# Kernel tuning notes

Hardware: AMD Instinct MI355X
Metric: run time of the kernel (lower is better)

## Reference

```python
import jax, jax.numpy as jnp
import numpy as np

B, D, H, C = 512, 1024, 512, 4


def setup_inputs() -> dict:
    key = jax.random.key(0)
    k_x, k_v, k_w = jax.random.split(key, 3)
    # x holds categorical values in [0, C) used as float multipliers
    x = jax.random.randint(k_x, (B, D), 0, C).astype(jnp.float32)
    # xavier_normal_ per torch fan computation: V fan_in=D*C, fan_out=H*C; W fan_in=D, fan_out=H
    V = jax.random.normal(k_v, (H, D, C), jnp.float32) * np.float32(np.sqrt(2.0 / (D * C + H * C)))
    b = jnp.zeros((D, C), jnp.float32)
    W = jax.random.normal(k_w, (H, D), jnp.float32) * np.float32(np.sqrt(2.0 / (D + H)))
    c = jnp.zeros((1, H), jnp.float32)
    return {"x": x, "V": V, "b": b, "W": W, "c": c}


def _nade_forward(x, V, b, W, c):
    Bsz = x.shape[0]
    a0 = jnp.broadcast_to(c, (Bsz, c.shape[1]))  # [B, H]
    # per-step slices stacked along leading D axis for lax.scan
    xs = (jnp.transpose(V, (1, 0, 2)),  # [D, H, C]
          b,                            # [D, C]
          W.T,                          # [D, H]
          x.T)                          # [D, B]

    def step(a, inp):
        V_d, b_d, w_d, x_d = inp
        h = jax.nn.sigmoid(a)                 # [B, H]
        logits = h @ V_d + b_d                # [B, C]
        p = jax.nn.log_softmax(logits, axis=1)
        a_new = a + x_d[:, None] * w_d[None, :]  # rank-1 update of running preactivation
        return a_new, (logits, p)

    _, (logits, p) = jax.lax.scan(step, a0, xs)   # each [D, B, C]
    y_hat = jnp.transpose(logits, (1, 0, 2)).reshape(Bsz, -1)  # [B, D*C], d-major blocks of size C
    p_hat = jnp.transpose(p, (1, 0, 2)).reshape(Bsz, -1)
    return y_hat, p_hat


def reference(x, V, b, W, c):
    return _nade_forward(x, V, b, W, c)
```

## Files before the change

### kernel.cpp

```cpp
#include <hip/hip_runtime.h>


#define Bv 512
#define Dv 1024
#define Hv 512
#define Cv 4
#define Kv 32
#define DCv 32

#define L2E 1.4426950408889634f
#define LN2 0.6931471805599453f

typedef __attribute__((ext_vector_type(8))) short short8;
typedef __attribute__((ext_vector_type(4))) float f32x4;

__device__ __forceinline__ float fexp2(float x) { return __builtin_amdgcn_exp2f(x); }
__device__ __forceinline__ float flog2(float x) { return __builtin_amdgcn_logf(x); }
__device__ __forceinline__ float frcp(float x)  { return __builtin_amdgcn_rcpf(x); }

__device__ __forceinline__ unsigned bf16pk(float lo, float hi) {
    return __builtin_amdgcn_perm(__float_as_uint(hi), __float_as_uint(lo), 0x07060302u);
}
__device__ __forceinline__ unsigned short bf16rne(float f) {
    unsigned u = __float_as_uint(f);
    return (unsigned short)((u + 0x7FFFu + ((u >> 16) & 1u)) >> 16);
}

__global__ __launch_bounds__(256) void k_prep(const float* __restrict__ W,
                                              const float* __restrict__ x,
                                              float* __restrict__ WtL,
                                              float* __restrict__ xt) {
    __shared__ float t[64][65];
    const int mb   = blockIdx.x >> 7;
    const int tile = blockIdx.x & 127;
    const int tr   = tile >> 4;
    const int tc   = tile & 15;
    const float* src = mb ? x : W;
    float* dst       = mb ? xt : WtL;
    const float scale = mb ? 1.0f : L2E;
    const int lx = threadIdx.x & 15;
    const int ly = threadIdx.x >> 4;

#pragma unroll
    for (int r = 0; r < 64; r += 16) {
        int row = r + ly;
        float4 v = *(const float4*)(src + (size_t)(tr * 64 + row) * Dv + tc * 64 + lx * 4);
        t[row][lx * 4 + 0] = v.x;
        t[row][lx * 4 + 1] = v.y;
        t[row][lx * 4 + 2] = v.z;
        t[row][lx * 4 + 3] = v.w;
    }
    __syncthreads();
#pragma unroll
    for (int r = 0; r < 64; r += 16) {
        int row = r + ly;
        float4 o = make_float4(t[lx * 4 + 0][row] * scale,
                               t[lx * 4 + 1][row] * scale,
                               t[lx * 4 + 2][row] * scale,
                               t[lx * 4 + 3][row] * scale);
        *(float4*)(dst + (size_t)(tc * 64 + row) * 512 + tr * 64 + lx * 4) = o;
    }
}

__global__ __launch_bounds__(256) void k_prepv(const float* __restrict__ V,
                                               unsigned short* __restrict__ VtA4) {
    __shared__ unsigned short tile[4 * 16 * 16 * 8];
    const int d0 = blockIdx.x * 4;
    const int dd = threadIdx.x & 3;
    const int hb0 = threadIdx.x >> 2;
#pragma unroll
    for (int p = 0; p < 8; ++p) {
        int h = p * 64 + hb0;
        float4 v = *(const float4*)(V + ((size_t)h * Dv + d0 + dd) * Cv);
        int hb = h >> 5, q = (h >> 3) & 3, j = h & 7;
        int base = ((dd * 16 + hb) * 16 + q * 4) * 8 + j;
        tile[base + 0 * 8] = bf16rne(v.x);
        tile[base + 1 * 8] = bf16rne(v.y);
        tile[base + 2 * 8] = bf16rne(v.z);
        tile[base + 3 * 8] = bf16rne(v.w);
    }
    __syncthreads();
    uint4* dst = (uint4*)(VtA4 + (size_t)d0 * 2048);
    const uint4* src = (const uint4*)tile;
    for (int tt = threadIdx.x; tt < 1024; tt += 256) dst[tt] = src[tt];
}

__global__ __launch_bounds__(512) void k_partial(const float* __restrict__ x,
                          const float* __restrict__ WtL, float* __restrict__ A0) {
    int k  = blockIdx.x >> 6;
    int bg = blockIdx.x & 63;
    int h  = threadIdx.x;
    int d0 = k * DCv;

    __shared__ float xs[DCv * 8];
    if (threadIdx.x < DCv * 8) {
        int g = threadIdx.x >> 5;
        int j = threadIdx.x & 31;
        xs[j * 8 + g] = x[(size_t)(bg * 8 + g) * Dv + d0 + j];
    }
    __syncthreads();

    float acc[8];
#pragma unroll
    for (int g = 0; g < 8; ++g) acc[g] = 0.0f;

    const float* wp = WtL + (size_t)d0 * Hv + h;
    for (int j = 0; j < DCv; ++j) {
        float wv = wp[(size_t)j * Hv];
        const float4 x0 = *(const float4*)(xs + j * 8);
        const float4 x1 = *(const float4*)(xs + j * 8 + 4);
        acc[0] = fmaf(x0.x, wv, acc[0]);
        acc[1] = fmaf(x0.y, wv, acc[1]);
        acc[2] = fmaf(x0.z, wv, acc[2]);
        acc[3] = fmaf(x0.w, wv, acc[3]);
        acc[4] = fmaf(x1.x, wv, acc[4]);
        acc[5] = fmaf(x1.y, wv, acc[5]);
        acc[6] = fmaf(x1.z, wv, acc[6]);
        acc[7] = fmaf(x1.w, wv, acc[7]);
    }
#pragma unroll
    for (int g = 0; g < 8; ++g)
        A0[((size_t)k * Bv + bg * 8 + g) * Hv + h] = acc[g];
}

__global__ void k_prefix(float* __restrict__ A0, const float* __restrict__ cbias) {
    int gid = blockIdx.x * blockDim.x + threadIdx.x;
    int h = gid & (Hv - 1);
    int bi = gid >> 9;
    float run = cbias[h] * L2E;
    float* p = A0 + (size_t)bi * Hv + h;
    for (int k = 0; k < Kv; ++k) {
        float t = p[(size_t)k * Bv * Hv];
        p[(size_t)k * Bv * Hv] = run;
        run += t;
    }
}

__global__ __launch_bounds__(256, 4) void k_main(
        const float* __restrict__ xt, const float* __restrict__ bbias,
        const unsigned short* __restrict__ VtA4, const float* __restrict__ WtL,
        const float* __restrict__ A0, float* __restrict__ out) {
    const int k    = blockIdx.x >> 5;
    const int bg   = blockIdx.x & 31;
    const int wid  = threadIdx.x >> 6;
    const int lane = threadIdx.x & 63;
    const int bl   = lane & 15;
    const int quad = lane >> 4;
    const int b    = bg * 16 + bl;
    const int d0   = k * DCv;
    const int stp  = wid >> 1;
    const bool isP = wid & 1;

    __shared__ f32x4 red[2][2][4][64];

    float a[32];
    {
        const float* ap = A0 + ((size_t)k * Bv + b) * Hv + wid * 128 + quad * 8;
#pragma unroll
        for (int kb = 0; kb < 4; ++kb) {
            float4 t0 = *(const float4*)(ap + kb * 32);
            float4 t1 = *(const float4*)(ap + kb * 32 + 4);
            a[kb*8+0]=t0.x; a[kb*8+1]=t0.y; a[kb*8+2]=t0.z; a[kb*8+3]=t0.w;
            a[kb*8+4]=t1.x; a[kb*8+5]=t1.y; a[kb*8+6]=t1.z; a[kb*8+7]=t1.w;
        }
    }

    const bool act = (bl < 4);
    const unsigned short* vp = VtA4 + (((size_t)d0 * 16 + wid * 4) * 16 + quad * 4 + bl) * 8;
    const float* wp = WtL + (size_t)d0 * Hv + wid * 128 + quad * 8;
    const float* xp = xt + (size_t)d0 * Bv + b;
    const float* bp = bbias + (d0 + stp) * Cv;
    float* sp = out + (isP ? (size_t)Bv * Dv * Cv : (size_t)0)
                    + (size_t)b * Dv * Cv + (d0 + stp) * Cv;

    const short8 zfrag = {0,0,0,0,0,0,0,0};

    for (int i1 = 0; i1 < DCv / 2; ++i1) {
        short8 afA[4], afB[4];
#pragma unroll
        for (int kb = 0; kb < 4; ++kb)
            afA[kb] = act ? *(const short8*)(vp + kb * 128) : zfrag;
#pragma unroll
        for (int kb = 0; kb < 4; ++kb)
            afB[kb] = act ? *(const short8*)(vp + 2048 + kb * 128) : zfrag;
        float xdA = xp[0];
        float xdB = xp[Bv];
        float4 bbv = *(const float4*)bp;

        unsigned pkA[16];
#pragma unroll
        for (int m = 0; m < 32; m += 2) {
            float s0 = frcp(1.0f + fexp2(-a[m]));
            float s1 = frcp(1.0f + fexp2(-a[m + 1]));
            pkA[m >> 1] = bf16pk(s0, s1);
        }
        f32x4 accA = {0.f, 0.f, 0.f, 0.f};
#pragma unroll
        for (int kb = 0; kb < 4; ++kb) {
            union { unsigned u[4]; short8 s; } cv;
            cv.u[0] = pkA[kb*4+0]; cv.u[1] = pkA[kb*4+1];
            cv.u[2] = pkA[kb*4+2]; cv.u[3] = pkA[kb*4+3];
            accA = __builtin_amdgcn_mfma_f32_16x16x32_bf16(afA[kb], cv.s, accA, 0, 0, 0);
        }
#pragma unroll
        for (int kb = 0; kb < 4; ++kb)
#pragma unroll
            for (int j = 0; j < 8; ++j)
                a[kb*8+j] = fmaf(xdA, wp[kb*32+j], a[kb*8+j]);

        unsigned pkB[16];
#pragma unroll
        for (int m = 0; m < 32; m += 2) {
            float s0 = frcp(1.0f + fexp2(-a[m]));
            float s1 = frcp(1.0f + fexp2(-a[m + 1]));
            pkB[m >> 1] = bf16pk(s0, s1);
        }
        f32x4 accB = {0.f, 0.f, 0.f, 0.f};
#pragma unroll
        for (int kb = 0; kb < 4; ++kb) {
            union { unsigned u[4]; short8 s; } cv;
            cv.u[0] = pkB[kb*4+0]; cv.u[1] = pkB[kb*4+1];
            cv.u[2] = pkB[kb*4+2]; cv.u[3] = pkB[kb*4+3];
            accB = __builtin_amdgcn_mfma_f32_16x16x32_bf16(afB[kb], cv.s, accB, 0, 0, 0);
        }
#pragma unroll
        for (int kb = 0; kb < 4; ++kb)
#pragma unroll
            for (int j = 0; j < 8; ++j)
                a[kb*8+j] = fmaf(xdB, wp[Hv + kb*32+j], a[kb*8+j]);

        red[i1 & 1][0][wid][lane] = accA;
        red[i1 & 1][1][wid][lane] = accB;
        __syncthreads();

        f32x4 r0 = red[i1 & 1][stp][0][lane];
        f32x4 r1 = red[i1 & 1][stp][1][lane];
        f32x4 r2 = red[i1 & 1][stp][2][lane];
        f32x4 r3 = red[i1 & 1][stp][3][lane];
        float w0 = r0.x + r1.x + r2.x + r3.x + bbv.x;
        float w1 = r0.y + r1.y + r2.y + r3.y + bbv.y;
        float w2 = r0.z + r1.z + r2.z + r3.z + bbv.z;
        float w3 = r0.w + r1.w + r2.w + r3.w + bbv.w;

        if (!isP) {
            if (quad == 0) *(float4*)sp = make_float4(w0, w1, w2, w3);
        } else {
            float mx = fmaxf(fmaxf(w0, w1), fmaxf(w2, w3));
            float e0 = fexp2((w0 - mx) * L2E);
            float e1 = fexp2((w1 - mx) * L2E);
            float e2 = fexp2((w2 - mx) * L2E);
            float e3 = fexp2((w3 - mx) * L2E);
            float lse = mx + flog2(e0 + e1 + e2 + e3) * LN2;
            if (quad == 0)
                *(float4*)sp = make_float4(w0 - lse, w1 - lse, w2 - lse, w3 - lse);
        }

        vp += 2 * 2048;
        wp += 2 * Hv;
        xp += 2 * Bv;
        bp += 2 * Cv;
        sp += 2 * Cv;
    }
}

extern "C" void kernel_launch(void* const* d_in, const int* in_sizes, int n_in,
                              void* d_out, int out_size, void* d_ws, size_t ws_size,
                              hipStream_t stream) {
    const float* x  = (const float*)d_in[0];
    const float* V  = (const float*)d_in[1];
    const float* bb = (const float*)d_in[2];
    const float* W  = (const float*)d_in[3];
    const float* cb = (const float*)d_in[4];
    float* out = (float*)d_out;

    char* ws = (char*)d_ws;
    unsigned short* VtA4 = (unsigned short*)ws;
    float* WtL = (float*)(ws + (size_t)4 * 1024 * 1024);
    float* xt  = (float*)(ws + (size_t)6 * 1024 * 1024);
    float* A0  = (float*)(ws + (size_t)8 * 1024 * 1024);

    k_prep<<<256, 256, 0, stream>>>(W, x, WtL, xt);
    k_prepv<<<Dv / 4, 256, 0, stream>>>(V, VtA4);
    k_partial<<<Kv * (Bv / 8), 512, 0, stream>>>(x, WtL, A0);
    k_prefix<<<(Bv * Hv) / 256, 256, 0, stream>>>(A0, cb);
    k_main<<<Kv * 32, 256, 0, stream>>>(xt, bb, VtA4, WtL, A0, out);
}
```

Baseline: 169.5 us.

## Merge prep kernels, fuse partial+prefix into one state kernel, widen main to 8 waves

Combines the W/x transpose and V repack into a single launch, and replaces the partial-sum plus prefix-scan kernels with one kernel that walks all chunks sequentially per batch group and writes running state directly. The main kernel now uses 512 threads with 8 waves, each owning 64 hidden units instead of 128. This halves per-thread register state and raises occupancy, and the packed float2 FMAs may lower instruction count. In exchange, the state kernel has only 64 blocks, which limits parallelism, and the cross-wave reduction now reads 8 partials instead of 4.

```diff
diff --git a/kernel.cpp b/kernel.cpp
--- a/kernel.cpp
+++ b/kernel.cpp
@@ -13,11 +13,20 @@
 
 typedef __attribute__((ext_vector_type(8))) short short8;
 typedef __attribute__((ext_vector_type(4))) float f32x4;
+typedef __attribute__((ext_vector_type(2))) float v2f;
 
 __device__ __forceinline__ float fexp2(float x) { return __builtin_amdgcn_exp2f(x); }
 __device__ __forceinline__ float flog2(float x) { return __builtin_amdgcn_logf(x); }
 __device__ __forceinline__ float frcp(float x)  { return __builtin_amdgcn_rcpf(x); }
 
+__device__ __forceinline__ v2f fma2(v2f a, v2f b, v2f c) {
+#if __has_builtin(__builtin_elementwise_fma)
+    return __builtin_elementwise_fma(a, b, c);
+#else
+    v2f r; r.x = fmaf(a.x, b.x, c.x); r.y = fmaf(a.y, b.y, c.y); return r;
+#endif
+}
+
 __device__ __forceinline__ unsigned bf16pk(float lo, float hi) {
     return __builtin_amdgcn_perm(__float_as_uint(hi), __float_as_uint(lo), 0x07060302u);
 }
@@ -26,117 +35,105 @@
     return (unsigned short)((u + 0x7FFFu + ((u >> 16) & 1u)) >> 16);
 }
 
-__global__ __launch_bounds__(256) void k_prep(const float* __restrict__ W,
-                                              const float* __restrict__ x,
-                                              float* __restrict__ WtL,
-                                              float* __restrict__ xt) {
-    __shared__ float t[64][65];
-    const int mb   = blockIdx.x >> 7;
-    const int tile = blockIdx.x & 127;
-    const int tr   = tile >> 4;
-    const int tc   = tile & 15;
-    const float* src = mb ? x : W;
-    float* dst       = mb ? xt : WtL;
-    const float scale = mb ? 1.0f : L2E;
-    const int lx = threadIdx.x & 15;
-    const int ly = threadIdx.x >> 4;
-
-#pragma unroll
-    for (int r = 0; r < 64; r += 16) {
-        int row = r + ly;
-        float4 v = *(const float4*)(src + (size_t)(tr * 64 + row) * Dv + tc * 64 + lx * 4);
-        t[row][lx * 4 + 0] = v.x;
-        t[row][lx * 4 + 1] = v.y;
-        t[row][lx * 4 + 2] = v.z;
-        t[row][lx * 4 + 3] = v.w;
+__global__ __launch_bounds__(256) void k_prep_all(
+        const float* __restrict__ V, const float* __restrict__ W,
+        const float* __restrict__ x, unsigned short* __restrict__ VtA4,
+        float* __restrict__ WtL, float* __restrict__ xt) {
+    __shared__ char smem[17408];
+    const int bid = blockIdx.x;
+    if (bid < 256) {
+        unsigned short* tile = (unsigned short*)smem;
+        const int d0 = bid * 4;
+        const int dd = threadIdx.x & 3;
+        const int hb0 = threadIdx.x >> 2;
+#pragma unroll
+        for (int p = 0; p < 8; ++p) {
+            int h = p * 64 + hb0;
+            float4 v = *(const float4*)(V + ((size_t)h * Dv + d0 + dd) * Cv);
+            int hb = h >> 5, q = (h >> 3) & 3, j = h & 7;
+            int base = ((dd * 16 + hb) * 16 + q * 4) * 8 + j;
+            tile[base + 0]  = bf16rne(v.x);
+            tile[base + 8]  = bf16rne(v.y);
+            tile[base + 16] = bf16rne(v.z);
+            tile[base + 24] = bf16rne(v.w);
+        }
+        __syncthreads();
+        uint4* dst = (uint4*)(VtA4 + (size_t)d0 * 2048);
+        const uint4* src = (const uint4*)tile;
+        for (int t = threadIdx.x; t < 1024; t += 256) dst[t] = src[t];
+    } else {
+        float (*t)[65] = (float (*)[65])smem;
+        const int mb   = (bid - 256) >> 7;
+        const int tile = (bid - 256) & 127;
+        const int tr   = tile >> 4;
+        const int tc   = tile & 15;
+        const float* src = mb ? x : W;
+        float* dst       = mb ? xt : WtL;
+        const float scale = mb ? 1.0f : L2E;
+        const int lx = threadIdx.x & 15;
+        const int ly = threadIdx.x >> 4;
+#pragma unroll
+        for (int r = 0; r < 64; r += 16) {
+            int row = r + ly;
+            float4 v = *(const float4*)(src + (size_t)(tr * 64 + row) * Dv + tc * 64 + lx * 4);
+            t[row][lx * 4 + 0] = v.x;
+            t[row][lx * 4 + 1] = v.y;
+            t[row][lx * 4 + 2] = v.z;
+            t[row][lx * 4 + 3] = v.w;
+        }
+        __syncthreads();
+#pragma unroll
+        for (int r = 0; r < 64; r += 16) {
+            int row = r + ly;
+            float4 o = make_float4(t[lx * 4 + 0][row] * scale,
+                                   t[lx * 4 + 1][row] * scale,
+                                   t[lx * 4 + 2][row] * scale,
+                                   t[lx * 4 + 3][row] * scale);
+            *(float4*)(dst + (size_t)(tc * 64 + row) * 512 + tr * 64 + lx * 4) = o;
+        }
+    }
+}
+
+__global__ __launch_bounds__(512) void k_state(
+        const float* __restrict__ x, const float* __restrict__ WtL,
+        const float* __restrict__ cb, float* __restrict__ A0) {
+    __shared__ float xs[Dv * 8];
+    const int bg = blockIdx.x;
+    const int h  = threadIdx.x;
+    for (int idx = threadIdx.x; idx < Dv * 8; idx += 512) {
+        int d = idx & (Dv - 1);
+        int g = idx >> 10;
+        xs[d * 8 + g] = x[(size_t)(bg * 8 + g) * Dv + d];
     }
     __syncthreads();
-#pragma unroll
-    for (int r = 0; r < 64; r += 16) {
-        int row = r + ly;
-        float4 o = make_float4(t[lx * 4 + 0][row] * scale,
-                               t[lx * 4 + 1][row] * scale,
-                               t[lx * 4 + 2][row] * scale,
-                               t[lx * 4 + 3][row] * scale);
-        *(float4*)(dst + (size_t)(tc * 64 + row) * 512 + tr * 64 + lx * 4) = o;
-    }
-}
-
-__global__ __launch_bounds__(256) void k_prepv(const float* __restrict__ V,
-                                               unsigned short* __restrict__ VtA4) {
-    __shared__ unsigned short tile[4 * 16 * 16 * 8];
-    const int d0 = blockIdx.x * 4;
-    const int dd = threadIdx.x & 3;
-    const int hb0 = threadIdx.x >> 2;
-#pragma unroll
-    for (int p = 0; p < 8; ++p) {
-        int h = p * 64 + hb0;
-        float4 v = *(const float4*)(V + ((size_t)h * Dv + d0 + dd) * Cv);
-        int hb = h >> 5, q = (h >> 3) & 3, j = h & 7;
-        int base = ((dd * 16 + hb) * 16 + q * 4) * 8 + j;
-        tile[base + 0 * 8] = bf16rne(v.x);
-        tile[base + 1 * 8] = bf16rne(v.y);
-        tile[base + 2 * 8] = bf16rne(v.z);
-        tile[base + 3 * 8] = bf16rne(v.w);
-    }
-    __syncthreads();
-    uint4* dst = (uint4*)(VtA4 + (size_t)d0 * 2048);
-    const uint4* src = (const uint4*)tile;
-    for (int tt = threadIdx.x; tt < 1024; tt += 256) dst[tt] = src[tt];
-}
-
-__global__ __launch_bounds__(512) void k_partial(const float* __restrict__ x,
-                          const float* __restrict__ WtL, float* __restrict__ A0) {
-    int k  = blockIdx.x >> 6;
-    int bg = blockIdx.x & 63;
-    int h  = threadIdx.x;
-    int d0 = k * DCv;
-
-    __shared__ float xs[DCv * 8];
-    if (threadIdx.x < DCv * 8) {
-        int g = threadIdx.x >> 5;
-        int j = threadIdx.x & 31;
-        xs[j * 8 + g] = x[(size_t)(bg * 8 + g) * Dv + d0 + j];
-    }
-    __syncthreads();
-
-    float acc[8];
-#pragma unroll
-    for (int g = 0; g < 8; ++g) acc[g] = 0.0f;
-
-    const float* wp = WtL + (size_t)d0 * Hv + h;
-    for (int j = 0; j < DCv; ++j) {
-        float wv = wp[(size_t)j * Hv];
-        const float4 x0 = *(const float4*)(xs + j * 8);
-        const float4 x1 = *(const float4*)(xs + j * 8 + 4);
-        acc[0] = fmaf(x0.x, wv, acc[0]);
-        acc[1] = fmaf(x0.y, wv, acc[1]);
-        acc[2] = fmaf(x0.z, wv, acc[2]);
-        acc[3] = fmaf(x0.w, wv, acc[3]);
-        acc[4] = fmaf(x1.x, wv, acc[4]);
-        acc[5] = fmaf(x1.y, wv, acc[5]);
-        acc[6] = fmaf(x1.z, wv, acc[6]);
-        acc[7] = fmaf(x1.w, wv, acc[7]);
-    }
-#pragma unroll
-    for (int g = 0; g < 8; ++g)
-        A0[((size_t)k * Bv + bg * 8 + g) * Hv + h] = acc[g];
-}
-
-__global__ void k_prefix(float* __restrict__ A0, const float* __restrict__ cbias) {
-    int gid = blockIdx.x * blockDim.x + threadIdx.x;
-    int h = gid & (Hv - 1);
-    int bi = gid >> 9;
-    float run = cbias[h] * L2E;
-    float* p = A0 + (size_t)bi * Hv + h;
-    for (int k = 0; k < Kv; ++k) {
-        float t = p[(size_t)k * Bv * Hv];
-        p[(size_t)k * Bv * Hv] = run;
-        run += t;
-    }
-}
-
-__global__ __launch_bounds__(256, 4) void k_main(
+    float cl = cb[h] * L2E;
+    v2f run[4];
+    run[0] = (v2f){cl, cl}; run[1] = (v2f){cl, cl};
+    run[2] = (v2f){cl, cl}; run[3] = (v2f){cl, cl};
+    const float* wp = WtL + h;
+    for (int kk = 0; kk < Kv; ++kk) {
+        float* a0p = A0 + ((size_t)kk * Bv + bg * 8) * Hv + h;
+#pragma unroll
+        for (int t = 0; t < 4; ++t) {
+            a0p[(size_t)(2 * t) * Hv]     = run[t].x;
+            a0p[(size_t)(2 * t + 1) * Hv] = run[t].y;
+        }
+        const float* wkk = wp + (size_t)kk * DCv * Hv;
+#pragma unroll 8
+        for (int j = 0; j < DCv; ++j) {
+            float wv = wkk[(size_t)j * Hv];
+            const float4 xa = *(const float4*)(xs + (kk * DCv + j) * 8);
+            const float4 xb = *(const float4*)(xs + (kk * DCv + j) * 8 + 4);
+            v2f wv2 = {wv, wv};
+            run[0] = fma2((v2f){xa.x, xa.y}, wv2, run[0]);
+            run[1] = fma2((v2f){xa.z, xa.w}, wv2, run[1]);
+            run[2] = fma2((v2f){xb.x, xb.y}, wv2, run[2]);
+            run[3] = fma2((v2f){xb.z, xb.w}, wv2, run[3]);
+        }
+    }
+}
+
+__global__ __launch_bounds__(512, 8) void k_main(
         const float* __restrict__ xt, const float* __restrict__ bbias,
         const unsigned short* __restrict__ VtA4, const float* __restrict__ WtL,
         const float* __restrict__ A0, float* __restrict__ out) {
@@ -148,111 +145,106 @@
     const int quad = lane >> 4;
     const int b    = bg * 16 + bl;
     const int d0   = k * DCv;
-    const int stp  = wid >> 1;
+    const int stp  = (wid >> 1) & 1;
     const bool isP = wid & 1;
-
-    __shared__ f32x4 red[2][2][4][64];
-
-    float a[32];
+    const bool active = wid < 4;
+
+    __shared__ f32x4 red[2][2][8][64];
+
+    v2f a2[8];
     {
-        const float* ap = A0 + ((size_t)k * Bv + b) * Hv + wid * 128 + quad * 8;
-#pragma unroll
-        for (int kb = 0; kb < 4; ++kb) {
-            float4 t0 = *(const float4*)(ap + kb * 32);
-            float4 t1 = *(const float4*)(ap + kb * 32 + 4);
-            a[kb*8+0]=t0.x; a[kb*8+1]=t0.y; a[kb*8+2]=t0.z; a[kb*8+3]=t0.w;
-            a[kb*8+4]=t1.x; a[kb*8+5]=t1.y; a[kb*8+6]=t1.z; a[kb*8+7]=t1.w;
-        }
-    }
-
-    const bool act = (bl < 4);
-    const unsigned short* vp = VtA4 + (((size_t)d0 * 16 + wid * 4) * 16 + quad * 4 + bl) * 8;
-    const float* wp = WtL + (size_t)d0 * Hv + wid * 128 + quad * 8;
+        const float* ap = A0 + ((size_t)k * Bv + b) * Hv + wid * 64 + quad * 8;
+#pragma unroll
+        for (int kb = 0; kb < 2; ++kb)
+#pragma unroll
+            for (int t = 0; t < 4; ++t)
+                a2[kb * 4 + t] = *(const v2f*)(ap + kb * 32 + 2 * t);
+    }
+
+    const int blc = (bl < 4) ? bl : 0;
+    const unsigned short* vp = VtA4 + (((size_t)d0 * 16 + wid * 2) * 16 + quad * 4 + blc) * 8;
+    const float* wp = WtL + (size_t)d0 * Hv + wid * 64 + quad * 8;
     const float* xp = xt + (size_t)d0 * Bv + b;
     const float* bp = bbias + (d0 + stp) * Cv;
     float* sp = out + (isP ? (size_t)Bv * Dv * Cv : (size_t)0)
                     + (size_t)b * Dv * Cv + (d0 + stp) * Cv;
 
-    const short8 zfrag = {0,0,0,0,0,0,0,0};
-
     for (int i1 = 0; i1 < DCv / 2; ++i1) {
-        short8 afA[4], afB[4];
-#pragma unroll
-        for (int kb = 0; kb < 4; ++kb)
-            afA[kb] = act ? *(const short8*)(vp + kb * 128) : zfrag;
-#pragma unroll
-        for (int kb = 0; kb < 4; ++kb)
-            afB[kb] = act ? *(const short8*)(vp + 2048 + kb * 128) : zfrag;
         float xdA = xp[0];
         float xdB = xp[Bv];
         float4 bbv = *(const float4*)bp;
 
-        unsigned pkA[16];
-#pragma unroll
-        for (int m = 0; m < 32; m += 2) {
-            float s0 = frcp(1.0f + fexp2(-a[m]));
-            float s1 = frcp(1.0f + fexp2(-a[m + 1]));
-            pkA[m >> 1] = bf16pk(s0, s1);
-        }
         f32x4 accA = {0.f, 0.f, 0.f, 0.f};
 #pragma unroll
-        for (int kb = 0; kb < 4; ++kb) {
+        for (int kb = 0; kb < 2; ++kb) {
             union { unsigned u[4]; short8 s; } cv;
-            cv.u[0] = pkA[kb*4+0]; cv.u[1] = pkA[kb*4+1];
-            cv.u[2] = pkA[kb*4+2]; cv.u[3] = pkA[kb*4+3];
-            accA = __builtin_amdgcn_mfma_f32_16x16x32_bf16(afA[kb], cv.s, accA, 0, 0, 0);
-        }
-#pragma unroll
-        for (int kb = 0; kb < 4; ++kb)
-#pragma unroll
-            for (int j = 0; j < 8; ++j)
-                a[kb*8+j] = fmaf(xdA, wp[kb*32+j], a[kb*8+j]);
-
-        unsigned pkB[16];
-#pragma unroll
-        for (int m = 0; m < 32; m += 2) {
-            float s0 = frcp(1.0f + fexp2(-a[m]));
-            float s1 = frcp(1.0f + fexp2(-a[m + 1]));
-            pkB[m >> 1] = bf16pk(s0, s1);
-        }
+#pragma unroll
+            for (int t = 0; t < 4; ++t) {
+                v2f aa = a2[kb * 4 + t];
+                v2f e; e.x = fexp2(-aa.x); e.y = fexp2(-aa.y);
+                v2f q = e + 1.0f;
+                cv.u[t] = bf16pk(frcp(q.x), frcp(q.y));
+            }
+            short8 af = *(const short8*)(vp + kb * 128);
+            accA = __builtin_amdgcn_mfma_f32_16x16x32_bf16(af, cv.s, accA, 0, 0, 0);
+        }
+        v2f xA2 = {xdA, xdA};
+#pragma unroll
+        for (int kb = 0; kb < 2; ++kb)
+#pragma unroll
+            for (int t = 0; t < 4; ++t) {
+                v2f wv = *(const v2f*)(wp + kb * 32 + 2 * t);
+                a2[kb * 4 + t] = fma2(xA2, wv, a2[kb * 4 + t]);
+            }
+
         f32x4 accB = {0.f, 0.f, 0.f, 0.f};
 #pragma unroll
-        for (int kb = 0; kb < 4; ++kb) {
+        for (int kb = 0; kb < 2; ++kb) {
             union { unsigned u[4]; short8 s; } cv;
-            cv.u[0] = pkB[kb*4+0]; cv.u[1] = pkB[kb*4+1];
-            cv.u[2] = pkB[kb*4+2]; cv.u[3] = pkB[kb*4+3];
-            accB = __builtin_amdgcn_mfma_f32_16x16x32_bf16(afB[kb], cv.s, accB, 0, 0, 0);
-        }
-#pragma unroll
-        for (int kb = 0; kb < 4; ++kb)
-#pragma unroll
-            for (int j = 0; j < 8; ++j)
-                a[kb*8+j] = fmaf(xdB, wp[Hv + kb*32+j], a[kb*8+j]);
+#pragma unroll
+            for (int t = 0; t < 4; ++t) {
+                v2f aa = a2[kb * 4 + t];
+                v2f e; e.x = fexp2(-aa.x); e.y = fexp2(-aa.y);
+                v2f q = e + 1.0f;
+                cv.u[t] = bf16pk(frcp(q.x), frcp(q.y));
+            }
+            short8 af = *(const short8*)(vp + 2048 + kb * 128);
+            accB = __builtin_amdgcn_mfma_f32_16x16x32_bf16(af, cv.s, accB, 0, 0, 0);
+        }
+        v2f xB2 = {xdB, xdB};
+#pragma unroll
+        for (int kb = 0; kb < 2; ++kb)
+#pragma unroll
+            for (int t = 0; t < 4; ++t) {
+                v2f wv = *(const v2f*)(wp + Hv + kb * 32 + 2 * t);
+                a2[kb * 4 + t] = fma2(xB2, wv, a2[kb * 4 + t]);
+            }
 
         red[i1 & 1][0][wid][lane] = accA;
         red[i1 & 1][1][wid][lane] = accB;
         __syncthreads();
 
-        f32x4 r0 = red[i1 & 1][stp][0][lane];
-        f32x4 r1 = red[i1 & 1][stp][1][lane];
-        f32x4 r2 = red[i1 & 1][stp][2][lane];
-        f32x4 r3 = red[i1 & 1][stp][3][lane];
-        float w0 = r0.x + r1.x + r2.x + r3.x + bbv.x;
-        float w1 = r0.y + r1.y + r2.y + r3.y + bbv.y;
-        float w2 = r0.z + r1.z + r2.z + r3.z + bbv.z;
-        float w3 = r0.w + r1.w + r2.w + r3.w + bbv.w;
-
-        if (!isP) {
-            if (quad == 0) *(float4*)sp = make_float4(w0, w1, w2, w3);
-        } else {
-            float mx = fmaxf(fmaxf(w0, w1), fmaxf(w2, w3));
-            float e0 = fexp2((w0 - mx) * L2E);
-            float e1 = fexp2((w1 - mx) * L2E);
-            float e2 = fexp2((w2 - mx) * L2E);
-            float e3 = fexp2((w3 - mx) * L2E);
-            float lse = mx + flog2(e0 + e1 + e2 + e3) * LN2;
-            if (quad == 0)
-                *(float4*)sp = make_float4(w0 - lse, w1 - lse, w2 - lse, w3 - lse);
+        if (active) {
+            f32x4 s = red[i1 & 1][stp][0][lane];
+#pragma unroll
+            for (int w8 = 1; w8 < 8; ++w8)
+                s += red[i1 & 1][stp][w8][lane];
+            float w0 = s.x + bbv.x;
+            float w1 = s.y + bbv.y;
+            float w2 = s.z + bbv.z;
+            float w3 = s.w + bbv.w;
+            if (!isP) {
+                if (quad == 0) *(float4*)sp = make_float4(w0, w1, w2, w3);
+            } else {
+                float mx = fmaxf(fmaxf(w0, w1), fmaxf(w2, w3));
+                float e0 = fexp2((w0 - mx) * L2E);
+                float e1 = fexp2((w1 - mx) * L2E);
+                float e2 = fexp2((w2 - mx) * L2E);
+                float e3 = fexp2((w3 - mx) * L2E);
+                float lse = mx + flog2(e0 + e1 + e2 + e3) * LN2;
+                if (quad == 0)
+                    *(float4*)sp = make_float4(w0 - lse, w1 - lse, w2 - lse, w3 - lse);
+            }
         }
 
         vp += 2 * 2048;
@@ -279,9 +271,7 @@
     float* xt  = (float*)(ws + (size_t)6 * 1024 * 1024);
     float* A0  = (float*)(ws + (size_t)8 * 1024 * 1024);
 
-    k_prep<<<256, 256, 0, stream>>>(W, x, WtL, xt);
-    k_prepv<<<Dv / 4, 256, 0, stream>>>(V, VtA4);
-    k_partial<<<Kv * (Bv / 8), 512, 0, stream>>>(x, WtL, A0);
-    k_prefix<<<(Bv * Hv) / 256, 256, 0, stream>>>(A0, cb);
-    k_main<<<Kv * 32, 256, 0, stream>>>(xt, bb, VtA4, WtL, A0, out);
-}
+    k_prep_all<<<512, 256, 0, stream>>>(V, W, x, VtA4, WtL, xt);
+    k_state<<<Bv / 8, 512, 0, stream>>>(x, WtL, cb, A0);
+    k_main<<<Kv * 32, 512, 0, stream>>>(xt, bb, VtA4, WtL, A0, out);
+}
```

Result: slower. 203.0 us (+19.8%).
